# Kernel optimization log

Measured on AMD Instinct MI355X. Metric: run time of the kernel, lower is better.

## Reference

```python
import jax, jax.numpy as jnp
import numpy as np

NUM_ITERATIONS = 3

def _squash(t, axis=-1):
    # norm here is the SQUARED norm, matching the torch code exactly
    norm = jnp.sum(t * t, axis=axis, keepdims=True)
    scale = norm / (1.0 + norm)
    return scale * t / jnp.sqrt(norm)

def setup_inputs() -> dict:
    key = jax.random.key(0)
    k1, k2 = jax.random.split(key)
    B, R, Cin = 1024, 2336, 4  # batch, num_routes, primary_capslen
    K, Cout = 2, 16            # num_caps, digital_capslen
    u = jax.random.normal(k1, (B, R, Cin), dtype=jnp.float32)
    W = jax.random.normal(k2, (K, R, Cin, Cout), dtype=jnp.float32)
    return {"u": u, "W": W}

def reference(u, W):
    # u: [B,R,Cin]; W: [K,R,Cin,Cout]
    # torch: u[:,None,:,None,:] @ W -> [B,K,R,1,Cout]; we drop the singleton.
    u_ji = jnp.einsum('bri,krio->bkro', u, W)  # [B,K,R,Cout]
    B, K, R, Cout = u_ji.shape
    # b is constant along the Cout axis (zeros init + delta_b keepdim), so keep it [B,K,R,1]
    b = jnp.zeros((B, K, R, 1), dtype=u_ji.dtype)
    v = None
    for i in range(NUM_ITERATIONS):
        c = jax.nn.softmax(b, axis=2)                      # softmax over routes (dim=2)
        s = jnp.sum(c * u_ji, axis=2, keepdims=True)       # [B,K,1,Cout]
        v = _squash(s, axis=-1)                            # [B,K,1,Cout]
        if i != NUM_ITERATIONS - 1:
            delta_b = jnp.sum(u_ji * v, axis=-1, keepdims=True)  # [B,K,R,1]
            b = b + delta_b
    v = jnp.squeeze(v, axis=2)                             # [B,K,Cout]
    classes = jnp.sqrt(jnp.sum(v * v, axis=-1))            # [B,K]
    return jax.nn.softmax(classes, axis=-1)                # F.softmax default dim=1 on 2D
```

## Files before the change

### kernel.cpp

```cpp
#include <hip/hip_runtime.h>
#include <stdint.h>

#define RT    2336
#define RLDS  1568
#define SCUT  12
#define NRS   6
#define NSL   13
#define NTH   512
#define NBLK  2048
#define BATCH 1024
#define SH1   32.0f
#define SH2   64.0f

__device__ __forceinline__ float blo(uint32_t v){ union {uint32_t u; float f;} x; x.u = v << 16;        return x.f; }
__device__ __forceinline__ float bhi(uint32_t v){ union {uint32_t u; float f;} x; x.u = v & 0xffff0000u; return x.f; }
__device__ __forceinline__ uint32_t f2b1(float f){
  union {float f; uint32_t u;} x; x.f = f;
  return (x.u + 0x7fffu + ((x.u >> 16) & 1u)) >> 16;
}
__device__ __forceinline__ uint32_t f2b_pack(float a, float b){ return f2b1(a) | (f2b1(b) << 16); }

__device__ __forceinline__ float qsum4(float d){
  d += __int_as_float(__builtin_amdgcn_update_dpp(
         0, __float_as_int(d), 0xB1, 0xF, 0xF, true));
  d += __int_as_float(__builtin_amdgcn_update_dpp(
         0, __float_as_int(d), 0x4E, 0xF, 0xF, true));
  return d;
}

__device__ __forceinline__ void merge_quad(float4& a, float l, int tid,
                                           float (*red)[4][5], float* vbuf,
                                           bool last, float* out_cls){
  #pragma unroll
  for (int off = 32; off >= 4; off >>= 1){
    a.x += __shfl_down(a.x, off); a.y += __shfl_down(a.y, off);
    a.z += __shfl_down(a.z, off); a.w += __shfl_down(a.w, off);
    l   += __shfl_down(l,   off);
  }
  const int lane = tid & 63, wid = tid >> 6;
  if (lane < 4){
    red[wid][lane][0] = l;
    red[wid][lane][1] = a.x; red[wid][lane][2] = a.y;
    red[wid][lane][3] = a.z; red[wid][lane][4] = a.w;
  }
  __syncthreads();
  if (tid < 16){
    const int q = tid >> 2, j = tid & 3;
    float S = 0.f, partL = 0.f;
    #pragma unroll
    for (int w = 0; w < 8; ++w){
      S     += red[w][q][1 + j];
      partL += red[w][j][0];
    }
    partL += __shfl_xor(partL, 1);
    partL += __shfl_xor(partL, 2);
    float L   = partL * 0.25f;
    float inv = 1.f / L;
    float Sn  = S * inv;
    float nrm = Sn * Sn;
    nrm += __shfl_xor(nrm, 1);
    nrm += __shfl_xor(nrm, 2);
    nrm += __shfl_xor(nrm, 4);
    nrm += __shfl_xor(nrm, 8);
    if (last){
      if (tid == 0) *out_cls = nrm / (1.f + nrm);
    } else {
      float f = sqrtf(nrm) / (1.f + nrm);
      vbuf[tid] = Sn * f;
    }
  }
  __syncthreads();
}

__global__ void __launch_bounds__(NTH, 4)
caps_route(const float* __restrict__ U, const float* __restrict__ W,
           float* __restrict__ Out){
  __shared__ uint2 uj[RLDS * 4];
  __shared__ float red[8][4][5];
  __shared__ float vbuf[16];

  const int tid = threadIdx.x;
  const int qo  = tid & 3;

  const int c  = blockIdx.x & 7;
  const int jj = blockIdx.x >> 3;
  const int k  = jj & 1;
  const int b  = (c << 7) | (jj >> 1);

  const float* Ub = U + (size_t)b * (RT * 4);
  const float* Wk = W + (size_t)k * ((size_t)RT * 64) + qo * 4;

  float4 acc; float l;
  float  ur[NRS][4];
  float  vc0, vc1, vc2, vc3;

  auto build_rq = [&](int route) -> float4 {
    float4 u4 = *(const float4*)(Ub + (size_t)route * 4);
    const float* wr = Wk + (size_t)route * 64;
    float4 w0 = *(const float4*)(wr);
    float4 w1 = *(const float4*)(wr + 16);
    float4 w2 = *(const float4*)(wr + 32);
    float4 w3 = *(const float4*)(wr + 48);
    float4 p;
    p.x = u4.x * w0.x; p.y = u4.x * w0.y; p.z = u4.x * w0.z; p.w = u4.x * w0.w;
    p.x = fmaf(u4.y, w1.x, p.x); p.y = fmaf(u4.y, w1.y, p.y);
    p.z = fmaf(u4.y, w1.z, p.z); p.w = fmaf(u4.y, w1.w, p.w);
    p.x = fmaf(u4.z, w2.x, p.x); p.y = fmaf(u4.z, w2.y, p.y);
    p.z = fmaf(u4.z, w2.z, p.z); p.w = fmaf(u4.z, w2.w, p.w);
    p.x = fmaf(u4.w, w3.x, p.x); p.y = fmaf(u4.w, w3.y, p.y);
    p.z = fmaf(u4.w, w3.z, p.z); p.w = fmaf(u4.w, w3.w, p.w);
    return p;
  };

  acc = make_float4(0.f, 0.f, 0.f, 0.f); l = 0.f;

  if (tid < 128){
    int route = tid >> 2;
    float4 p = build_rq(route);
    acc.x += p.x; acc.y += p.y; acc.z += p.z; acc.w += p.w; l += 1.f;
    uj[route*4 + qo] = make_uint2(f2b_pack(p.x, p.y), f2b_pack(p.z, p.w));
  }
  #pragma unroll 3
  for (int s = 0; s < SCUT; ++s){
    int route = 32 + s*128 + (tid >> 2);
    float4 p = build_rq(route);
    acc.x += p.x; acc.y += p.y; acc.z += p.z; acc.w += p.w; l += 1.f;
    uj[route*4 + qo] = make_uint2(f2b_pack(p.x, p.y), f2b_pack(p.z, p.w));
  }
  #pragma unroll
  for (int slot = 0; slot < NRS; ++slot){
    int route = 32 + (SCUT + slot)*128 + (tid >> 2);
    float4 p = build_rq(route);
    acc.x += p.x; acc.y += p.y; acc.z += p.z; acc.w += p.w; l += 1.f;
    ur[slot][0] = p.x; ur[slot][1] = p.y; ur[slot][2] = p.z; ur[slot][3] = p.w;
  }
  merge_quad(acc, l, tid, red, vbuf, false, nullptr);
  vc0 = vbuf[4*qo]; vc1 = vbuf[4*qo+1]; vc2 = vbuf[4*qo+2]; vc3 = vbuf[4*qo+3];

  acc = make_float4(0.f, 0.f, 0.f, 0.f); l = 0.f;
  #pragma unroll
  for (int s = 0; s < NSL; ++s){
    int idx = tid + (s << 9);
    bool act = (idx < RLDS * 4);
    float uf0=0.f, uf1=0.f, uf2=0.f, uf3=0.f, d = 0.f;
    if (act){
      uint2 q2 = uj[idx];
      uf0 = blo(q2.x); uf1 = bhi(q2.x); uf2 = blo(q2.y); uf3 = bhi(q2.y);
      d = fmaf(uf0, vc0, fmaf(uf1, vc1, fmaf(uf2, vc2, uf3 * vc3)));
    }
    d = qsum4(d);
    if (act){
      float e = __expf(d - SH1);
      l += e;
      acc.x = fmaf(e, uf0, acc.x); acc.y = fmaf(e, uf1, acc.y);
      acc.z = fmaf(e, uf2, acc.z); acc.w = fmaf(e, uf3, acc.w);
    }
  }
  #pragma unroll
  for (int slot = 0; slot < NRS; ++slot){
    float d = fmaf(ur[slot][0], vc0, fmaf(ur[slot][1], vc1,
              fmaf(ur[slot][2], vc2, ur[slot][3] * vc3)));
    d = qsum4(d);
    float e = __expf(d - SH1);
    l += e;
    acc.x = fmaf(e, ur[slot][0], acc.x); acc.y = fmaf(e, ur[slot][1], acc.y);
    acc.z = fmaf(e, ur[slot][2], acc.z); acc.w = fmaf(e, ur[slot][3], acc.w);
  }
  merge_quad(acc, l, tid, red, vbuf, false, nullptr);
  vc0 += vbuf[4*qo]; vc1 += vbuf[4*qo+1]; vc2 += vbuf[4*qo+2]; vc3 += vbuf[4*qo+3];

  acc = make_float4(0.f, 0.f, 0.f, 0.f); l = 0.f;
  #pragma unroll
  for (int s = 0; s < NSL; ++s){
    int idx = tid + (s << 9);
    bool act = (idx < RLDS * 4);
    float uf0=0.f, uf1=0.f, uf2=0.f, uf3=0.f, d = 0.f;
    if (act){
      uint2 q2 = uj[idx];
      uf0 = blo(q2.x); uf1 = bhi(q2.x); uf2 = blo(q2.y); uf3 = bhi(q2.y);
      d = fmaf(uf0, vc0, fmaf(uf1, vc1, fmaf(uf2, vc2, uf3 * vc3)));
    }
    d = qsum4(d);
    if (act){
      float e = __expf(d - SH2);
      l += e;
      acc.x = fmaf(e, uf0, acc.x); acc.y = fmaf(e, uf1, acc.y);
      acc.z = fmaf(e, uf2, acc.z); acc.w = fmaf(e, uf3, acc.w);
    }
  }
  #pragma unroll
  for (int slot = 0; slot < NRS; ++slot){
    float d = fmaf(ur[slot][0], vc0, fmaf(ur[slot][1], vc1,
              fmaf(ur[slot][2], vc2, ur[slot][3] * vc3)));
    d = qsum4(d);
    float e = __expf(d - SH2);
    l += e;
    acc.x = fmaf(e, ur[slot][0], acc.x); acc.y = fmaf(e, ur[slot][1], acc.y);
    acc.z = fmaf(e, ur[slot][2], acc.z); acc.w = fmaf(e, ur[slot][3], acc.w);
  }
  merge_quad(acc, l, tid, red, vbuf, true, Out + ((b << 1) | k));
}

__global__ void caps_softmax(float* __restrict__ Out){
  int b = blockIdx.x * blockDim.x + threadIdx.x;
  if (b < BATCH){
    float2* p = (float2*)Out;
    float2 c = p[b];
    float m  = fmaxf(c.x, c.y);
    float e0 = __expf(c.x - m), e1 = __expf(c.y - m);
    float inv = 1.f / (e0 + e1);
    p[b] = make_float2(e0 * inv, e1 * inv);
  }
}

extern "C" void kernel_launch(void* const* d_in, const int* in_sizes, int n_in,
                              void* d_out, int out_size, void* d_ws, size_t ws_size,
                              hipStream_t stream) {
  const float* U = (const float*)d_in[0];
  const float* W = (const float*)d_in[1];
  float* Out = (float*)d_out;
  caps_route<<<dim3(NBLK), dim3(NTH), 0, stream>>>(U, W, Out);
  caps_softmax<<<dim3(BATCH / 256), dim3(256), 0, stream>>>(Out);
}
```

Measured before the change: 140.9 us.

## Process two batch rows per block to reuse W loads across batches

Each block now handles two batch elements sharing the same capsule k, so every W row loaded from global memory feeds two u_ji computations. Blocks are halved, and LDS holds bf16 u_ji for both batches with fewer routes each. The register-resident tail is stored packed as bf16 instead of fp32. Occupancy drops to two blocks per CU, and the tail routes lose precision from bf16 packing.

```diff
diff --git a/kernel.cpp b/kernel.cpp
--- a/kernel.cpp
+++ b/kernel.cpp
@@ -2,12 +2,11 @@
 #include <stdint.h>
 
 #define RT    2336
-#define RLDS  1568
-#define SCUT  12
-#define NRS   6
-#define NSL   13
+#define RL    1184
+#define NSL2  10
+#define NRS2  9
 #define NTH   512
-#define NBLK  2048
+#define NBLK  1024
 #define BATCH 1024
 #define SH1   32.0f
 #define SH2   64.0f
@@ -19,6 +18,9 @@
   return (x.u + 0x7fffu + ((x.u >> 16) & 1u)) >> 16;
 }
 __device__ __forceinline__ uint32_t f2b_pack(float a, float b){ return f2b1(a) | (f2b1(b) << 16); }
+__device__ __forceinline__ uint2 pack4(float4 p){
+  return make_uint2(f2b_pack(p.x, p.y), f2b_pack(p.z, p.w));
+}
 
 __device__ __forceinline__ float qsum4(float d){
   d += __int_as_float(__builtin_amdgcn_update_dpp(
@@ -28,29 +30,36 @@
   return d;
 }
 
-__device__ __forceinline__ void merge_quad(float4& a, float l, int tid,
-                                           float (*red)[4][5], float* vbuf,
-                                           bool last, float* out_cls){
+__device__ __forceinline__ void merge2(float4 aA, float lA, float4 aB, float lB,
+                                       int tid, float (*red)[8][4][5],
+                                       float (*vbuf)[16],
+                                       bool last, float* outp){
   #pragma unroll
   for (int off = 32; off >= 4; off >>= 1){
-    a.x += __shfl_down(a.x, off); a.y += __shfl_down(a.y, off);
-    a.z += __shfl_down(a.z, off); a.w += __shfl_down(a.w, off);
-    l   += __shfl_down(l,   off);
+    aA.x += __shfl_down(aA.x, off); aA.y += __shfl_down(aA.y, off);
+    aA.z += __shfl_down(aA.z, off); aA.w += __shfl_down(aA.w, off);
+    lA   += __shfl_down(lA,   off);
+    aB.x += __shfl_down(aB.x, off); aB.y += __shfl_down(aB.y, off);
+    aB.z += __shfl_down(aB.z, off); aB.w += __shfl_down(aB.w, off);
+    lB   += __shfl_down(lB,   off);
   }
   const int lane = tid & 63, wid = tid >> 6;
   if (lane < 4){
-    red[wid][lane][0] = l;
-    red[wid][lane][1] = a.x; red[wid][lane][2] = a.y;
-    red[wid][lane][3] = a.z; red[wid][lane][4] = a.w;
+    red[0][wid][lane][0] = lA;
+    red[0][wid][lane][1] = aA.x; red[0][wid][lane][2] = aA.y;
+    red[0][wid][lane][3] = aA.z; red[0][wid][lane][4] = aA.w;
+    red[1][wid][lane][0] = lB;
+    red[1][wid][lane][1] = aB.x; red[1][wid][lane][2] = aB.y;
+    red[1][wid][lane][3] = aB.z; red[1][wid][lane][4] = aB.w;
   }
   __syncthreads();
-  if (tid < 16){
-    const int q = tid >> 2, j = tid & 3;
+  if (tid < 32){
+    const int bt = tid >> 4, t = tid & 15, q = t >> 2, j = t & 3;
     float S = 0.f, partL = 0.f;
     #pragma unroll
     for (int w = 0; w < 8; ++w){
-      S     += red[w][q][1 + j];
-      partL += red[w][j][0];
+      S     += red[bt][w][q][1 + j];
+      partL += red[bt][w][j][0];
     }
     partL += __shfl_xor(partL, 1);
     partL += __shfl_xor(partL, 2);
@@ -63,142 +72,147 @@
     nrm += __shfl_xor(nrm, 4);
     nrm += __shfl_xor(nrm, 8);
     if (last){
-      if (tid == 0) *out_cls = nrm / (1.f + nrm);
+      if (t == 0) outp[bt << 1] = nrm / (1.f + nrm);
     } else {
       float f = sqrtf(nrm) / (1.f + nrm);
-      vbuf[tid] = Sn * f;
+      vbuf[bt][t] = Sn * f;
     }
   }
   __syncthreads();
 }
 
-__global__ void __launch_bounds__(NTH, 4)
+__global__ void __launch_bounds__(NTH, 2)
 caps_route(const float* __restrict__ U, const float* __restrict__ W,
            float* __restrict__ Out){
-  __shared__ uint2 uj[RLDS * 4];
-  __shared__ float red[8][4][5];
-  __shared__ float vbuf[16];
+  __shared__ uint2 uj[2][RL * 4];
+  __shared__ float red[2][8][4][5];
+  __shared__ float vbuf[2][16];
 
   const int tid = threadIdx.x;
   const int qo  = tid & 3;
 
-  const int c  = blockIdx.x & 7;
-  const int jj = blockIdx.x >> 3;
-  const int k  = jj & 1;
-  const int b  = (c << 7) | (jj >> 1);
-
-  const float* Ub = U + (size_t)b * (RT * 4);
-  const float* Wk = W + (size_t)k * ((size_t)RT * 64) + qo * 4;
-
-  float4 acc; float l;
-  float  ur[NRS][4];
-  float  vc0, vc1, vc2, vc3;
-
-  auto build_rq = [&](int route) -> float4 {
-    float4 u4 = *(const float4*)(Ub + (size_t)route * 4);
+  const int c    = blockIdx.x & 7;
+  const int jj   = blockIdx.x >> 3;
+  const int k    = jj & 1;
+  const int pair = (c << 6) | (jj >> 1);
+  const int bb   = pair << 1;
+
+  const float* Ub0 = U + (size_t)bb * (RT * 4);
+  const float* Ub1 = Ub0 + (RT * 4);
+  const float* Wk  = W + (size_t)k * ((size_t)RT * 64) + qo * 4;
+
+  float4 accA, accB; float lA, lB;
+  uint2  ura[NRS2], urb[NRS2];
+  float  vA0, vA1, vA2, vA3, vB0, vB1, vB2, vB3;
+
+  auto build2 = [&](int route, float4& pa, float4& pb){
+    float4 ua = *(const float4*)(Ub0 + (size_t)route * 4);
+    float4 ub = *(const float4*)(Ub1 + (size_t)route * 4);
     const float* wr = Wk + (size_t)route * 64;
     float4 w0 = *(const float4*)(wr);
     float4 w1 = *(const float4*)(wr + 16);
     float4 w2 = *(const float4*)(wr + 32);
     float4 w3 = *(const float4*)(wr + 48);
-    float4 p;
-    p.x = u4.x * w0.x; p.y = u4.x * w0.y; p.z = u4.x * w0.z; p.w = u4.x * w0.w;
-    p.x = fmaf(u4.y, w1.x, p.x); p.y = fmaf(u4.y, w1.y, p.y);
-    p.z = fmaf(u4.y, w1.z, p.z); p.w = fmaf(u4.y, w1.w, p.w);
-    p.x = fmaf(u4.z, w2.x, p.x); p.y = fmaf(u4.z, w2.y, p.y);
-    p.z = fmaf(u4.z, w2.z, p.z); p.w = fmaf(u4.z, w2.w, p.w);
-    p.x = fmaf(u4.w, w3.x, p.x); p.y = fmaf(u4.w, w3.y, p.y);
-    p.z = fmaf(u4.w, w3.z, p.z); p.w = fmaf(u4.w, w3.w, p.w);
-    return p;
+    pa.x = ua.x * w0.x; pa.y = ua.x * w0.y; pa.z = ua.x * w0.z; pa.w = ua.x * w0.w;
+    pa.x = fmaf(ua.y, w1.x, pa.x); pa.y = fmaf(ua.y, w1.y, pa.y);
+    pa.z = fmaf(ua.y, w1.z, pa.z); pa.w = fmaf(ua.y, w1.w, pa.w);
+    pa.x = fmaf(ua.z, w2.x, pa.x); pa.y = fmaf(ua.z, w2.y, pa.y);
+    pa.z = fmaf(ua.z, w2.z, pa.z); pa.w = fmaf(ua.z, w2.w, pa.w);
+    pa.x = fmaf(ua.w, w3.x, pa.x); pa.y = fmaf(ua.w, w3.y, pa.y);
+    pa.z = fmaf(ua.w, w3.z, pa.z); pa.w = fmaf(ua.w, w3.w, pa.w);
+    pb.x = ub.x * w0.x; pb.y = ub.x * w0.y; pb.z = ub.x * w0.z; pb.w = ub.x * w0.w;
+    pb.x = fmaf(ub.y, w1.x, pb.x); pb.y = fmaf(ub.y, w1.y, pb.y);
+    pb.z = fmaf(ub.y, w1.z, pb.z); pb.w = fmaf(ub.y, w1.w, pb.w);
+    pb.x = fmaf(ub.z, w2.x, pb.x); pb.y = fmaf(ub.z, w2.y, pb.y);
+    pb.z = fmaf(ub.z, w2.z, pb.z); pb.w = fmaf(ub.z, w2.w, pb.w);
+    pb.x = fmaf(ub.w, w3.x, pb.x); pb.y = fmaf(ub.w, w3.y, pb.y);
+    pb.z = fmaf(ub.w, w3.z, pb.z); pb.w = fmaf(ub.w, w3.w, pb.w);
   };
 
-  acc = make_float4(0.f, 0.f, 0.f, 0.f); l = 0.f;
+  accA = make_float4(0.f,0.f,0.f,0.f); accB = make_float4(0.f,0.f,0.f,0.f);
+  lA = 0.f; lB = 0.f;
 
   if (tid < 128){
     int route = tid >> 2;
-    float4 p = build_rq(route);
-    acc.x += p.x; acc.y += p.y; acc.z += p.z; acc.w += p.w; l += 1.f;
-    uj[route*4 + qo] = make_uint2(f2b_pack(p.x, p.y), f2b_pack(p.z, p.w));
+    float4 pa, pb; build2(route, pa, pb);
+    accA.x += pa.x; accA.y += pa.y; accA.z += pa.z; accA.w += pa.w; lA += 1.f;
+    accB.x += pb.x; accB.y += pb.y; accB.z += pb.z; accB.w += pb.w; lB += 1.f;
+    uj[0][route*4 + qo] = pack4(pa);
+    uj[1][route*4 + qo] = pack4(pb);
   }
   #pragma unroll 3
-  for (int s = 0; s < SCUT; ++s){
+  for (int s = 0; s < 9; ++s){
     int route = 32 + s*128 + (tid >> 2);
-    float4 p = build_rq(route);
-    acc.x += p.x; acc.y += p.y; acc.z += p.z; acc.w += p.w; l += 1.f;
-    uj[route*4 + qo] = make_uint2(f2b_pack(p.x, p.y), f2b_pack(p.z, p.w));
+    float4 pa, pb; build2(route, pa, pb);
+    accA.x += pa.x; accA.y += pa.y; accA.z += pa.z; accA.w += pa.w; lA += 1.f;
+    accB.x += pb.x; accB.y += pb.y; accB.z += pb.z; accB.w += pb.w; lB += 1.f;
+    uj[0][route*4 + qo] = pack4(pa);
+    uj[1][route*4 + qo] = pack4(pb);
   }
   #pragma unroll
-  for (int slot = 0; slot < NRS; ++slot){
-    int route = 32 + (SCUT + slot)*128 + (tid >> 2);
-    float4 p = build_rq(route);
-    acc.x += p.x; acc.y += p.y; acc.z += p.z; acc.w += p.w; l += 1.f;
-    ur[slot][0] = p.x; ur[slot][1] = p.y; ur[slot][2] = p.z; ur[slot][3] = p.w;
-  }
-  merge_quad(acc, l, tid, red, vbuf, false, nullptr);
-  vc0 = vbuf[4*qo]; vc1 = vbuf[4*qo+1]; vc2 = vbuf[4*qo+2]; vc3 = vbuf[4*qo+3];
-
-  acc = make_float4(0.f, 0.f, 0.f, 0.f); l = 0.f;
-  #pragma unroll
-  for (int s = 0; s < NSL; ++s){
-    int idx = tid + (s << 9);
-    bool act = (idx < RLDS * 4);
-    float uf0=0.f, uf1=0.f, uf2=0.f, uf3=0.f, d = 0.f;
-    if (act){
-      uint2 q2 = uj[idx];
-      uf0 = blo(q2.x); uf1 = bhi(q2.x); uf2 = blo(q2.y); uf3 = bhi(q2.y);
-      d = fmaf(uf0, vc0, fmaf(uf1, vc1, fmaf(uf2, vc2, uf3 * vc3)));
-    }
-    d = qsum4(d);
-    if (act){
-      float e = __expf(d - SH1);
-      l += e;
-      acc.x = fmaf(e, uf0, acc.x); acc.y = fmaf(e, uf1, acc.y);
-      acc.z = fmaf(e, uf2, acc.z); acc.w = fmaf(e, uf3, acc.w);
-    }
-  }
-  #pragma unroll
-  for (int slot = 0; slot < NRS; ++slot){
-    float d = fmaf(ur[slot][0], vc0, fmaf(ur[slot][1], vc1,
-              fmaf(ur[slot][2], vc2, ur[slot][3] * vc3)));
-    d = qsum4(d);
-    float e = __expf(d - SH1);
-    l += e;
-    acc.x = fmaf(e, ur[slot][0], acc.x); acc.y = fmaf(e, ur[slot][1], acc.y);
-    acc.z = fmaf(e, ur[slot][2], acc.z); acc.w = fmaf(e, ur[slot][3], acc.w);
-  }
-  merge_quad(acc, l, tid, red, vbuf, false, nullptr);
-  vc0 += vbuf[4*qo]; vc1 += vbuf[4*qo+1]; vc2 += vbuf[4*qo+2]; vc3 += vbuf[4*qo+3];
-
-  acc = make_float4(0.f, 0.f, 0.f, 0.f); l = 0.f;
-  #pragma unroll
-  for (int s = 0; s < NSL; ++s){
-    int idx = tid + (s << 9);
-    bool act = (idx < RLDS * 4);
-    float uf0=0.f, uf1=0.f, uf2=0.f, uf3=0.f, d = 0.f;
-    if (act){
-      uint2 q2 = uj[idx];
-      uf0 = blo(q2.x); uf1 = bhi(q2.x); uf2 = blo(q2.y); uf3 = bhi(q2.y);
-      d = fmaf(uf0, vc0, fmaf(uf1, vc1, fmaf(uf2, vc2, uf3 * vc3)));
-    }
-    d = qsum4(d);
-    if (act){
-      float e = __expf(d - SH2);
-      l += e;
-      acc.x = fmaf(e, uf0, acc.x); acc.y = fmaf(e, uf1, acc.y);
-      acc.z = fmaf(e, uf2, acc.z); acc.w = fmaf(e, uf3, acc.w);
-    }
-  }
-  #pragma unroll
-  for (int slot = 0; slot < NRS; ++slot){
-    float d = fmaf(ur[slot][0], vc0, fmaf(ur[slot][1], vc1,
-              fmaf(ur[slot][2], vc2, ur[slot][3] * vc3)));
-    d = qsum4(d);
-    float e = __expf(d - SH2);
-    l += e;
-    acc.x = fmaf(e, ur[slot][0], acc.x); acc.y = fmaf(e, ur[slot][1], acc.y);
-    acc.z = fmaf(e, ur[slot][2], acc.z); acc.w = fmaf(e, ur[slot][3], acc.w);
-  }
-  merge_quad(acc, l, tid, red, vbuf, true, Out + ((b << 1) | k));
+  for (int slot = 0; slot < NRS2; ++slot){
+    int route = RL + slot*128 + (tid >> 2);
+    float4 pa, pb; build2(route, pa, pb);
+    accA.x += pa.x; accA.y += pa.y; accA.z += pa.z; accA.w += pa.w; lA += 1.f;
+    accB.x += pb.x; accB.y += pb.y; accB.z += pb.z; accB.w += pb.w; lB += 1.f;
+    ura[slot] = pack4(pa);
+    urb[slot] = pack4(pb);
+  }
+  merge2(accA, lA, accB, lB, tid, red, vbuf, false, nullptr);
+  vA0 = vbuf[0][4*qo]; vA1 = vbuf[0][4*qo+1]; vA2 = vbuf[0][4*qo+2]; vA3 = vbuf[0][4*qo+3];
+  vB0 = vbuf[1][4*qo]; vB1 = vbuf[1][4*qo+1]; vB2 = vbuf[1][4*qo+2]; vB3 = vbuf[1][4*qo+3];
+
+  for (int ps = 0; ps < 2; ++ps){
+    const float SH = ps ? SH2 : SH1;
+    accA = make_float4(0.f,0.f,0.f,0.f); accB = make_float4(0.f,0.f,0.f,0.f);
+    lA = 0.f; lB = 0.f;
+    #pragma unroll
+    for (int s = 0; s < NSL2; ++s){
+      int idx = tid + (s << 9);
+      bool act = (idx < RL * 4);
+      float a0=0.f,a1=0.f,a2=0.f,a3=0.f, c0=0.f,c1=0.f,c2=0.f,c3=0.f;
+      float dA = 0.f, dB = 0.f;
+      if (act){
+        uint2 qa = uj[0][idx], qb = uj[1][idx];
+        a0 = blo(qa.x); a1 = bhi(qa.x); a2 = blo(qa.y); a3 = bhi(qa.y);
+        c0 = blo(qb.x); c1 = bhi(qb.x); c2 = blo(qb.y); c3 = bhi(qb.y);
+        dA = fmaf(a0, vA0, fmaf(a1, vA1, fmaf(a2, vA2, a3 * vA3)));
+        dB = fmaf(c0, vB0, fmaf(c1, vB1, fmaf(c2, vB2, c3 * vB3)));
+      }
+      dA = qsum4(dA); dB = qsum4(dB);
+      if (act){
+        float eA = __expf(dA - SH), eB = __expf(dB - SH);
+        lA += eA; lB += eB;
+        accA.x = fmaf(eA, a0, accA.x); accA.y = fmaf(eA, a1, accA.y);
+        accA.z = fmaf(eA, a2, accA.z); accA.w = fmaf(eA, a3, accA.w);
+        accB.x = fmaf(eB, c0, accB.x); accB.y = fmaf(eB, c1, accB.y);
+        accB.z = fmaf(eB, c2, accB.z); accB.w = fmaf(eB, c3, accB.w);
+      }
+    }
+    #pragma unroll
+    for (int slot = 0; slot < NRS2; ++slot){
+      uint2 qa = ura[slot], qb = urb[slot];
+      float a0 = blo(qa.x), a1 = bhi(qa.x), a2 = blo(qa.y), a3 = bhi(qa.y);
+      float c0 = blo(qb.x), c1 = bhi(qb.x), c2 = blo(qb.y), c3 = bhi(qb.y);
+      float dA = fmaf(a0, vA0, fmaf(a1, vA1, fmaf(a2, vA2, a3 * vA3)));
+      float dB = fmaf(c0, vB0, fmaf(c1, vB1, fmaf(c2, vB2, c3 * vB3)));
+      dA = qsum4(dA); dB = qsum4(dB);
+      float eA = __expf(dA - SH), eB = __expf(dB - SH);
+      lA += eA; lB += eB;
+      accA.x = fmaf(eA, a0, accA.x); accA.y = fmaf(eA, a1, accA.y);
+      accA.z = fmaf(eA, a2, accA.z); accA.w = fmaf(eA, a3, accA.w);
+      accB.x = fmaf(eB, c0, accB.x); accB.y = fmaf(eB, c1, accB.y);
+      accB.z = fmaf(eB, c2, accB.z); accB.w = fmaf(eB, c3, accB.w);
+    }
+    merge2(accA, lA, accB, lB, tid, red, vbuf, ps == 1,
+           Out + (bb << 1) + k);
+    if (ps == 0){
+      vA0 += vbuf[0][4*qo]; vA1 += vbuf[0][4*qo+1];
+      vA2 += vbuf[0][4*qo+2]; vA3 += vbuf[0][4*qo+3];
+      vB0 += vbuf[1][4*qo]; vB1 += vbuf[1][4*qo+1];
+      vB2 += vbuf[1][4*qo+2]; vB3 += vbuf[1][4*qo+3];
+    }
+  }
 }
 
 __global__ void caps_softmax(float* __restrict__ Out){
```

Measured after the change: 133.2 us. 5.5% less time.
